# Kernel tuning notes

Hardware: AMD Instinct MI355X
Metric: run time of the kernel (lower is better)

The kernel has to match this reference:

```python
import jax, jax.numpy as jnp
import numpy as np

D_MODEL = 1024
N_HEADS = 16
D_K = D_MODEL // N_HEADS
BATCH = 4
SEQ = 2048


def setup_inputs() -> dict:
    key = jax.random.key(0)
    ks = jax.random.split(key, 9)
    s = 1.0 / np.sqrt(D_MODEL)
    x = jax.random.normal(ks[0], (BATCH, SEQ, D_MODEL), dtype=jnp.float32)
    # nn.Linear weights stored as [out, in]; we keep [in, out] for x @ W
    Wq = jax.random.uniform(ks[1], (D_MODEL, D_MODEL), jnp.float32, -s, s)
    bq = jax.random.uniform(ks[2], (D_MODEL,), jnp.float32, -s, s)
    Wk = jax.random.uniform(ks[3], (D_MODEL, D_MODEL), jnp.float32, -s, s)
    bk = jax.random.uniform(ks[4], (D_MODEL,), jnp.float32, -s, s)
    Wv = jax.random.uniform(ks[5], (D_MODEL, D_MODEL), jnp.float32, -s, s)
    bv = jax.random.uniform(ks[6], (D_MODEL,), jnp.float32, -s, s)
    Wo = jax.random.uniform(ks[7], (D_MODEL, D_MODEL), jnp.float32, -s, s)
    bo = jax.random.uniform(ks[8], (D_MODEL,), jnp.float32, -s, s)
    return {"x": x, "Wq": Wq, "bq": bq, "Wk": Wk, "bk": bk,
            "Wv": Wv, "bv": bv, "Wo": Wo, "bo": bo}


def reference(x, Wq, bq, Wk, bk, Wv, bv, Wo, bo):
    B, S, _ = x.shape
    # projections -> [B, H, S, d_k]
    def heads(t):
        return t.reshape(B, S, N_HEADS, D_K).transpose(0, 2, 1, 3)
    q = heads(x @ Wq + bq)
    k = heads(x @ Wk + bk)
    v = heads(x @ Wv + bv)
    scores = jnp.einsum('bhqd,bhkd->bhqk', q, k) / jnp.sqrt(jnp.float32(D_K))
    causal = jnp.tril(jnp.ones((S, S), dtype=bool))
    scores = jnp.where(causal[None, None], scores, -jnp.inf)
    attn = jax.nn.softmax(scores, axis=-1)  # dropout p=0 (eval) -> identity
    out = jnp.einsum('bhqk,bhkd->bhqd', attn, v)
    out = out.transpose(0, 2, 1, 3).reshape(B, S, D_MODEL)
    return out @ Wo + bo
```

## Files before the change

kernel.cpp:

```cpp
#include <hip/hip_runtime.h>
#include <hip/hip_bf16.h>
#include <stdint.h>

#define D_MODEL 1024
#define N_HEADS 16
#define D_KH    64
#define BATCH   4
#define SEQ     2048
#define M_TOTAL (BATCH * SEQ)

typedef unsigned short u16;
typedef short  bf16x8 __attribute__((ext_vector_type(8)));
typedef float  f32x4  __attribute__((ext_vector_type(4)));

__device__ __forceinline__ float bf2f(u16 u) {
    union { uint32_t i; float f; } c; c.i = ((uint32_t)u) << 16; return c.f;
}
__device__ __forceinline__ u16 f2bf(float f) {
    union { float f; uint32_t i; } c; c.f = f;
    uint32_t r = (c.i + 0x7FFFu + ((c.i >> 16) & 1u)) >> 16;
    return (u16)r;
}
__device__ __forceinline__ uint32_t cvt_pk_bf16(float lo, float hi) {
    uint32_t r;
    asm("v_cvt_pk_bf16_f32 %0, %1, %2" : "=v"(r) : "v"(lo), "v"(hi));
    return r;
}
__device__ __forceinline__ float sane(float v) {
    return (v == v && v > -1e30f && v < 1e30f) ? v : 0.f;
}
__device__ __forceinline__ float loadf(const void* base, size_t idx, int isbf) {
    return isbf ? bf2f(((const u16*)base)[idx]) : ((const float*)base)[idx];
}
__device__ __forceinline__ void gload16(const void* g, void* lds) {
    __builtin_amdgcn_global_load_lds(
        (const __attribute__((address_space(1))) void*)g,
        (__attribute__((address_space(3))) void*)lds, 16, 0, 0);
}

__global__ void detect_dtype(const uint32_t* __restrict__ w, int* __restrict__ flag) {
    uint32_t word = w[threadIdx.x & 63];
    uint32_t e = (word >> 7) & 0xFFu;
    unsigned long long m = __ballot(e >= 64u && e <= 160u);
    if (threadIdx.x == 0) *flag = (__popcll(m) >= 48) ? 1 : 0;
}

__global__ __launch_bounds__(256) void convert_x(
    const void* __restrict__ x, u16* __restrict__ dst, const int* __restrict__ flag)
{
    if (*flag) return;
    size_t i = ((size_t)blockIdx.x * 256 + threadIdx.x) * 8;
    const float* f = (const float*)x + i;
    float4 a = *(const float4*)f;
    float4 b = *(const float4*)(f + 4);
    union { ushort4 v; u16 s[4]; } lo, hi;
    lo.s[0] = f2bf(a.x); lo.s[1] = f2bf(a.y); lo.s[2] = f2bf(a.z); lo.s[3] = f2bf(a.w);
    hi.s[0] = f2bf(b.x); hi.s[1] = f2bf(b.y); hi.s[2] = f2bf(b.z); hi.s[3] = f2bf(b.w);
    *(ushort4*)&dst[i]     = lo.v;
    *(ushort4*)&dst[i + 4] = hi.v;
}

__global__ __launch_bounds__(256) void transpose_w(
    const void* __restrict__ W0, const void* __restrict__ W1,
    const void* __restrict__ W2, u16* __restrict__ dst,
    const int* __restrict__ flag)
{
    const int mat = blockIdx.z;
    const void* W = (mat == 0) ? W0 : ((mat == 1) ? W1 : W2);
    const int isbf = *flag;
    const int n0 = blockIdx.x << 6, k0 = blockIdx.y << 6;
    __shared__ u16 Ts[64 * 72];
    const int t = threadIdx.x;
    const int rr = t >> 4, cc = (t & 15) << 2;

#pragma unroll
    for (int i = 0; i < 4; i++) {
        int row = rr + i * 16;
        if (isbf) {
            ushort4 v = *(const ushort4*)((const u16*)W + (size_t)(k0 + row) * D_MODEL + n0 + cc);
            *(ushort4*)&Ts[row * 72 + cc] = v;
        } else {
            float4 f = *(const float4*)((const float*)W + (size_t)(k0 + row) * D_MODEL + n0 + cc);
            Ts[row * 72 + cc + 0] = f2bf(f.x);
            Ts[row * 72 + cc + 1] = f2bf(f.y);
            Ts[row * 72 + cc + 2] = f2bf(f.z);
            Ts[row * 72 + cc + 3] = f2bf(f.w);
        }
    }
    __syncthreads();
#pragma unroll
    for (int i = 0; i < 4; i++) {
        int n = rr + i * 16;
        union { ushort4 v; u16 s[4]; } o;
        o.s[0] = Ts[(cc + 0) * 72 + n];
        o.s[1] = Ts[(cc + 1) * 72 + n];
        o.s[2] = Ts[(cc + 2) * 72 + n];
        o.s[3] = Ts[(cc + 3) * 72 + n];
        *(ushort4*)&dst[(size_t)mat * 1048576 + (size_t)(n0 + n) * D_MODEL + k0 + cc] = o.v;
    }
}

__global__ __launch_bounds__(256) void qkv_gemm(
    const void* __restrict__ Xorig, const u16* __restrict__ Xbf,
    const u16* __restrict__ Wt,
    const void* __restrict__ bq, const void* __restrict__ bk, const void* __restrict__ bv,
    u16* __restrict__ Qd, u16* __restrict__ Kw, u16* __restrict__ Vt,
    const int* __restrict__ flag)
{
    const int isbf = *flag;
    const u16* Xp = isbf ? (const u16*)Xorig : Xbf;

    const int tid = threadIdx.x;
    const int wave = tid >> 6, lane = tid & 63;
    const int quad = lane >> 4, l15 = lane & 15;
    const int wr = wave >> 1, wc = wave & 1;

    const int nt  = blockIdx.x;
    const int mat = nt >> 3;
    const int n0m = (nt & 7) << 7;
    const int m0  = blockIdx.y << 7;

    const u16* Wmat = Wt + (size_t)mat * 1048576;
    const void* bias = (mat == 0) ? bq : ((mat == 1) ? bk : bv);

    __shared__ __align__(16) u16 As[128 * 36];
    __shared__ __align__(16) u16 Bs[128 * 36];

    f32x4 acc[4][4];
#pragma unroll
    for (int i = 0; i < 4; i++)
#pragma unroll
        for (int j = 0; j < 4; j++) acc[i][j] = (f32x4){0.f, 0.f, 0.f, 0.f};

    for (int k0 = 0; k0 < D_MODEL; k0 += 32) {
#pragma unroll
        for (int i = 0; i < 2; i++) {
            int c = tid + (i << 8);
            int row = c >> 2, koff = (c & 3) << 3;
            *(uint4*)&As[row * 36 + koff] =
                *(const uint4*)&Xp[(size_t)(m0 + row) * D_MODEL + k0 + koff];
            *(uint4*)&Bs[row * 36 + koff] =
                *(const uint4*)&Wmat[(size_t)(n0m + row) * D_MODEL + k0 + koff];
        }
        __syncthreads();

        bf16x8 af[4], bf[4];
#pragma unroll
        for (int ms = 0; ms < 4; ms++)
            af[ms] = *(const bf16x8*)&As[(wr * 64 + ms * 16 + l15) * 36 + quad * 8];
#pragma unroll
        for (int ns = 0; ns < 4; ns++)
            bf[ns] = *(const bf16x8*)&Bs[(wc * 64 + ns * 16 + l15) * 36 + quad * 8];
#pragma unroll
        for (int ms = 0; ms < 4; ms++)
#pragma unroll
            for (int ns = 0; ns < 4; ns++)
                acc[ms][ns] = __builtin_amdgcn_mfma_f32_16x16x32_bf16(af[ms], bf[ns], acc[ms][ns], 0, 0, 0);
        __syncthreads();
    }

#pragma unroll
    for (int ns = 0; ns < 4; ns++) {
        int c = n0m + wc * 64 + ns * 16 + l15;
        float bv_ = loadf(bias, c, isbf);
        int h = c >> 6, d = c & 63;
#pragma unroll
        for (int ms = 0; ms < 4; ms++) {
            int rbase = m0 + wr * 64 + ms * 16 + quad * 4;
            int b = rbase >> 11;
            int sbase = rbase & 2047;
            int bh = b * N_HEADS + h;
            if (mat == 2) {
                union { ushort4 v; u16 s[4]; } o;
#pragma unroll
                for (int r = 0; r < 4; r++) o.s[r] = f2bf(sane(acc[ms][ns][r] + bv_));
                *(ushort4*)&Vt[((size_t)bh * D_KH + d) * SEQ + sbase] = o.v;
            } else {
                u16* Out = (mat == 0) ? Qd : Kw;
#pragma unroll
                for (int r = 0; r < 4; r++)
                    Out[((size_t)bh * SEQ + sbase + r) * D_KH + d] =
                        f2bf(sane(acc[ms][ns][r] + bv_));
            }
        }
    }
}

__global__ __launch_bounds__(256, 2) void attn_kernel(
    const u16* __restrict__ Qd, const u16* __restrict__ Kw,
    const u16* __restrict__ Vt, u16* __restrict__ Aw)
{
    const int tid = threadIdx.x;
    const int wave = tid >> 6, lane = tid & 63;
    const int quad = lane >> 4, l15 = lane & 15;

    const int bh = blockIdx.x;
    const int p  = blockIdx.y;
    const int b  = bh >> 4, h = bh & 15;

    const u16* Qb = Qd + (size_t)bh * SEQ * D_KH;
    const char* Kb = (const char*)(Kw + (size_t)bh * SEQ * D_KH);
    const char* Vb = (const char*)(Vt + (size_t)bh * D_KH * SEQ);

    __shared__ __align__(16) u16 KV[2][8192];
    __shared__ __align__(16) u16 Ps[4][32 * 64];
    char* Pw = (char*)Ps[wave];

    const float CEXP = 0.18033688011112042f;

    const int lrow = lane >> 3;
    const int gchk = (lane & 7) ^ lrow;
    const int hxor = l15 & 7;

    for (int ph = 0; ph < 2; ph++) {
        const int qt = ph ? (15 - p) : p;
        const int qrow0 = qt * 128 + wave * 32;

        bf16x8 qf[2][2];
#pragma unroll
        for (int qs = 0; qs < 2; qs++) {
            const u16* qrow = Qb + (size_t)(qrow0 + qs * 16 + l15) * D_KH + quad * 8;
            qf[qs][0] = *(const bf16x8*)(qrow);
            qf[qs][1] = *(const bf16x8*)(qrow + 32);
        }

        float mi[2], li[2];
        f32x4 od[4][2];
        mi[0] = mi[1] = -1e9f; li[0] = li[1] = 0.f;
#pragma unroll
        for (int db = 0; db < 4; db++)
#pragma unroll
            for (int qs = 0; qs < 2; qs++) od[db][qs] = (f32x4){0.f, 0.f, 0.f, 0.f};

        const int ktn = 2 * qt + 2;

        auto stage_issue = [&](int k0, int buf) {
            char* kb = (char*)KV[buf];
#pragma unroll
            for (int j = 0; j < 2; j++) {
                const int r0 = 16 * wave + 8 * j;
                gload16(Kb + (size_t)(k0 + r0 + lrow) * 128 + 16 * gchk,
                        kb + r0 * 128);
                gload16(Vb + (size_t)(r0 + lrow) * 4096 + (size_t)k0 * 2 + 16 * gchk,
                        kb + 8192 + r0 * 128);
            }
        };

        stage_issue(0, 0);
        __syncthreads();

        int cur = 0;
        for (int kt = 0; kt < ktn; ++kt) {
            const int k0 = kt << 6;
            const bool pf = (kt + 1 < ktn);

            if (pf) stage_issue(k0 + 64, cur ^ 1);

            const char* kb = (const char*)KV[cur];

            bf16x8 kf[4][2];
#pragma unroll
            for (int nb = 0; nb < 4; nb++) {
                const char* kr = kb + (nb * 16 + l15) * 128;
                kf[nb][0] = *(const bf16x8*)(kr + 16 * (quad ^ hxor));
                kf[nb][1] = *(const bf16x8*)(kr + 16 * ((4 + quad) ^ hxor));
            }

            f32x4 st[4][2];
#pragma unroll
            for (int nb = 0; nb < 4; nb++)
#pragma unroll
                for (int qs = 0; qs < 2; qs++) {
                    f32x4 t = (f32x4){0.f, 0.f, 0.f, 0.f};
                    t = __builtin_amdgcn_mfma_f32_16x16x32_bf16(kf[nb][0], qf[qs][0], t, 0, 0, 0);
                    t = __builtin_amdgcn_mfma_f32_16x16x32_bf16(kf[nb][1], qf[qs][1], t, 0, 0, 0);
                    st[nb][qs] = t;
                }

            if (kt >= 2 * qt) {
#pragma unroll
                for (int qs = 0; qs < 2; qs++) {
                    const int q = qrow0 + qs * 16 + l15;
#pragma unroll
                    for (int nb = 0; nb < 4; nb++) {
                        const int kb0 = k0 + nb * 16 + quad * 4;
#pragma unroll
                        for (int r = 0; r < 4; r++)
                            if (kb0 + r > q) st[nb][qs][r] = -1e9f;
                    }
                }
            }

#pragma unroll
            for (int qs = 0; qs < 2; qs++) {
                float a0 = fmaxf(fmaxf(st[0][qs][0], st[0][qs][1]), fmaxf(st[0][qs][2], st[0][qs][3]));
                float a1 = fmaxf(fmaxf(st[1][qs][0], st[1][qs][1]), fmaxf(st[1][qs][2], st[1][qs][3]));
                float a2 = fmaxf(fmaxf(st[2][qs][0], st[2][qs][1]), fmaxf(st[2][qs][2], st[2][qs][3]));
                float a3 = fmaxf(fmaxf(st[3][qs][0], st[3][qs][1]), fmaxf(st[3][qs][2], st[3][qs][3]));
                float pmax = fmaxf(fmaxf(a0, a1), fmaxf(a2, a3));
                pmax = fmaxf(pmax, __shfl_xor(pmax, 16, 64));
                pmax = fmaxf(pmax, __shfl_xor(pmax, 32, 64));
                if (__any(pmax > mi[qs] + 8.0f)) {
                    float mnew  = fmaxf(mi[qs], pmax);
                    float alpha = exp2f((mi[qs] - mnew) * CEXP);
                    mi[qs] = mnew;
                    li[qs] *= alpha;
#pragma unroll
                    for (int db = 0; db < 4; db++) {
                        od[db][qs][0] *= alpha; od[db][qs][1] *= alpha;
                        od[db][qs][2] *= alpha; od[db][qs][3] *= alpha;
                    }
                }
                const float mc = mi[qs] * CEXP;
                float srow_ = 0.f;
#pragma unroll
                for (int nb = 0; nb < 4; nb++) {
                    float pf0 = exp2f(fmaf(st[nb][qs][0], CEXP, -mc));
                    float pf1 = exp2f(fmaf(st[nb][qs][1], CEXP, -mc));
                    float pf2 = exp2f(fmaf(st[nb][qs][2], CEXP, -mc));
                    float pf3 = exp2f(fmaf(st[nb][qs][3], CEXP, -mc));
                    srow_ += (pf0 + pf1) + (pf2 + pf3);
                    union { uint2 w; ushort4 v; } pk;
                    pk.w.x = cvt_pk_bf16(pf0, pf1);
                    pk.w.y = cvt_pk_bf16(pf2, pf3);
                    const int sw = (4 * nb + quad) ^ ((l15 & 7) << 1);
                    *(uint2*)(Pw + (qs * 16 + l15) * 128 + sw * 8) = pk.w;
                }
                srow_ += __shfl_xor(srow_, 16, 64);
                srow_ += __shfl_xor(srow_, 32, 64);
                li[qs] += srow_;
            }

            bf16x8 pa[2][2];
#pragma unroll
            for (int qs = 0; qs < 2; qs++)
#pragma unroll
                for (int j = 0; j < 2; j++) {
                    const int mw = (4 * j + quad) ^ (l15 & 7);
                    pa[qs][j] = *(const bf16x8*)(Pw + (qs * 16 + l15) * 128 + mw * 16);
                }

#pragma unroll
            for (int db = 0; db < 4; db++) {
                const char* vr = kb + 8192 + (db * 16 + l15) * 128;
                bf16x8 v0 = *(const bf16x8*)(vr + 16 * (quad ^ hxor));
                bf16x8 v1 = *(const bf16x8*)(vr + 16 * ((4 + quad) ^ hxor));
#pragma unroll
                for (int qs = 0; qs < 2; qs++) {
                    od[db][qs] = __builtin_amdgcn_mfma_f32_16x16x32_bf16(v0, pa[qs][0], od[db][qs], 0, 0, 0);
                    od[db][qs] = __builtin_amdgcn_mfma_f32_16x16x32_bf16(v1, pa[qs][1], od[db][qs], 0, 0, 0);
                }
            }

            __syncthreads();
            cur ^= 1;
        }

#pragma unroll
        for (int qs = 0; qs < 2; qs++) {
            const int q = qrow0 + qs * 16 + l15;
            const float inv = 1.0f / fmaxf(li[qs], 1e-30f);
            u16* orow = Aw + (size_t)(b * SEQ + q) * D_MODEL + h * D_KH;
#pragma unroll
            for (int db = 0; db < 4; db++)
#pragma unroll
                for (int r = 0; r < 4; r++)
                    orow[db * 16 + quad * 4 + r] = f2bf(sane(od[db][qs][r] * inv));
        }
        __syncthreads();
    }
}

__global__ __launch_bounds__(256) void out_gemm(
    const u16* __restrict__ A, const u16* __restrict__ Wot,
    const void* __restrict__ bias, void* __restrict__ Out,
    const int* __restrict__ flag)
{
    const int isbf = *flag;
    const int tid = threadIdx.x;
    const int wave = tid >> 6, lane = tid & 63;
    const int quad = lane >> 4, l15 = lane & 15;
    const int wr = wave >> 1, wc = wave & 1;

    const int n0 = blockIdx.x << 7;
    const int m0 = blockIdx.y << 7;

    __shared__ __align__(16) u16 As[128 * 36];
    __shared__ __align__(16) u16 Bs[128 * 36];

    f32x4 acc[4][4];
#pragma unroll
    for (int i = 0; i < 4; i++)
#pragma unroll
        for (int j = 0; j < 4; j++) acc[i][j] = (f32x4){0.f, 0.f, 0.f, 0.f};

    for (int k0 = 0; k0 < D_MODEL; k0 += 32) {
#pragma unroll
        for (int i = 0; i < 2; i++) {
            int c = tid + (i << 8);
            int row = c >> 2, koff = (c & 3) << 3;
            *(uint4*)&As[row * 36 + koff] =
                *(const uint4*)&A[(size_t)(m0 + row) * D_MODEL + k0 + koff];
            *(uint4*)&Bs[row * 36 + koff] =
                *(const uint4*)&Wot[(size_t)(n0 + row) * D_MODEL + k0 + koff];
        }
        __syncthreads();

        bf16x8 af[4], bf[4];
#pragma unroll
        for (int ms = 0; ms < 4; ms++)
            af[ms] = *(const bf16x8*)&As[(wr * 64 + ms * 16 + l15) * 36 + quad * 8];
#pragma unroll
        for (int ns = 0; ns < 4; ns++)
            bf[ns] = *(const bf16x8*)&Bs[(wc * 64 + ns * 16 + l15) * 36 + quad * 8];
#pragma unroll
        for (int ms = 0; ms < 4; ms++)
#pragma unroll
            for (int ns = 0; ns < 4; ns++)
                acc[ms][ns] = __builtin_amdgcn_mfma_f32_16x16x32_bf16(af[ms], bf[ns], acc[ms][ns], 0, 0, 0);
        __syncthreads();
    }

#pragma unroll
    for (int ns = 0; ns < 4; ns++) {
        int col = n0 + wc * 64 + ns * 16 + l15;
        float bv_ = loadf(bias, col, isbf);
#pragma unroll
        for (int ms = 0; ms < 4; ms++) {
#pragma unroll
            for (int r = 0; r < 4; r++) {
                int row = m0 + wr * 64 + ms * 16 + quad * 4 + r;
                float v = sane(acc[ms][ns][r] + bv_);
                size_t idx = (size_t)row * D_MODEL + col;
                if (isbf) ((u16*)Out)[idx] = f2bf(v);
                else      ((float*)Out)[idx] = v;
            }
        }
    }
}

__global__ void zero_out_kernel(void* out, int n, const int* flag) {
    int i = blockIdx.x * 256 + threadIdx.x;
    if (i < n) {
        if (*flag) ((u16*)out)[i] = 0;
        else       ((float*)out)[i] = 0.f;
    }
}

extern "C" void kernel_launch(void* const* d_in, const int* in_sizes, int n_in,
                              void* d_out, int out_size, void* d_ws, size_t ws_size,
                              hipStream_t stream)
{
    const void* x  = d_in[0];
    const void* Wq = d_in[1];
    const void* bq = d_in[2];
    const void* Wk = d_in[3];
    const void* bk = d_in[4];
    const void* Wv = d_in[5];
    const void* bv = d_in[6];
    const void* Wo = d_in[7];
    const void* bo = d_in[8];

    const size_t NELT = (size_t)M_TOTAL * D_MODEL;
    const size_t HDR  = 4096;
    const size_t NEED = HDR + 3 * NELT * sizeof(u16);

    int* flag = (int*)d_ws;
    detect_dtype<<<1, 64, 0, stream>>>((const uint32_t*)Wq, flag);

    if (ws_size < NEED) {
        zero_out_kernel<<<(out_size + 255) / 256, 256, 0, stream>>>(d_out, out_size, flag);
        return;
    }

    u16* base = (u16*)((char*)d_ws + HDR);
    u16* Kw      = base;
    u16* Vt      = base + NELT;
    u16* Wo_t    = Vt;
    u16* Wqkv_t  = base + 2 * NELT;
    u16* Aw      = base + 2 * NELT;
    u16* Qd      = (u16*)d_out;
    u16* Xbf     = (u16*)d_out + NELT;

    convert_x<<<dim3(M_TOTAL * D_MODEL / (8 * 256)), 256, 0, stream>>>(x, Xbf, flag);
    transpose_w<<<dim3(16, 16, 3), 256, 0, stream>>>(Wq, Wk, Wv, Wqkv_t, flag);

    qkv_gemm<<<dim3(24, 64), 256, 0, stream>>>(x, Xbf, Wqkv_t, bq, bk, bv,
                                               Qd, Kw, Vt, flag);
    attn_kernel<<<dim3(64, 8), 256, 0, stream>>>(Qd, Kw, Vt, Aw);
    transpose_w<<<dim3(16, 16, 1), 256, 0, stream>>>(Wo, Wo, Wo, Wo_t, flag);
    out_gemm<<<dim3(8, 64), 256, 0, stream>>>(Aw, Wo_t, bo, d_out, flag);
}
```

Baseline: 313.5 us.

## Double-buffer GEMM tiles with direct global-to-LDS loads and XOR swizzle

Both the QKV and output-projection GEMMs now use a double-buffered LDS pipeline with a K-tile of 64. The next tile is fetched with gload16 (global-to-LDS loads) while MFMAs run on the current one, and an XOR swizzle replaces the padded layout to avoid bank conflicts. This removes one barrier per step and the register round-trip for staging, aiming to overlap memory latency with compute. The cost is LDS use rising to 64KB per block, and the launch bound now asks for 2 blocks per CU.

```diff
diff --git a/kernel.cpp b/kernel.cpp
--- a/kernel.cpp
+++ b/kernel.cpp
@@ -100,7 +100,7 @@
     }
 }
 
-__global__ __launch_bounds__(256) void qkv_gemm(
+__global__ __launch_bounds__(256, 2) void qkv_gemm(
     const void* __restrict__ Xorig, const u16* __restrict__ Xbf,
     const u16* __restrict__ Wt,
     const void* __restrict__ bq, const void* __restrict__ bk, const void* __restrict__ bv,
@@ -123,8 +123,25 @@
     const u16* Wmat = Wt + (size_t)mat * 1048576;
     const void* bias = (mat == 0) ? bq : ((mat == 1) ? bk : bv);
 
-    __shared__ __align__(16) u16 As[128 * 36];
-    __shared__ __align__(16) u16 Bs[128 * 36];
+    __shared__ __align__(16) u16 As[2][128 * 64];
+    __shared__ __align__(16) u16 Bs[2][128 * 64];
+
+    const int lrow = lane >> 3;
+    const int gchk = (lane & 7) ^ lrow;
+    const int hxor = l15 & 7;
+
+    auto stage = [&](int k0, int buf) {
+        char* ap = (char*)As[buf];
+        char* bp = (char*)Bs[buf];
+#pragma unroll
+        for (int j = 0; j < 4; j++) {
+            const int r0 = 32 * wave + 8 * j;
+            gload16((const char*)Xp   + ((size_t)(m0  + r0 + lrow) * D_MODEL + k0) * 2 + 16 * gchk,
+                    ap + r0 * 128);
+            gload16((const char*)Wmat + ((size_t)(n0m + r0 + lrow) * D_MODEL + k0) * 2 + 16 * gchk,
+                    bp + r0 * 128);
+        }
+    };
 
     f32x4 acc[4][4];
 #pragma unroll
@@ -132,31 +149,36 @@
 #pragma unroll
         for (int j = 0; j < 4; j++) acc[i][j] = (f32x4){0.f, 0.f, 0.f, 0.f};
 
-    for (int k0 = 0; k0 < D_MODEL; k0 += 32) {
-#pragma unroll
-        for (int i = 0; i < 2; i++) {
-            int c = tid + (i << 8);
-            int row = c >> 2, koff = (c & 3) << 3;
-            *(uint4*)&As[row * 36 + koff] =
-                *(const uint4*)&Xp[(size_t)(m0 + row) * D_MODEL + k0 + koff];
-            *(uint4*)&Bs[row * 36 + koff] =
-                *(const uint4*)&Wmat[(size_t)(n0m + row) * D_MODEL + k0 + koff];
+    stage(0, 0);
+    __syncthreads();
+
+    int cur = 0;
+    for (int kt = 0; kt < 16; ++kt) {
+        if (kt + 1 < 16) stage((kt + 1) * 64, cur ^ 1);
+
+        const char* ap = (const char*)As[cur];
+        const char* bp = (const char*)Bs[cur];
+#pragma unroll
+        for (int kk = 0; kk < 2; kk++) {
+            bf16x8 af[4], bf[4];
+#pragma unroll
+            for (int ms = 0; ms < 4; ms++) {
+                const char* ar = ap + (wr * 64 + ms * 16 + l15) * 128;
+                af[ms] = *(const bf16x8*)(ar + 16 * ((4 * kk + quad) ^ hxor));
+            }
+#pragma unroll
+            for (int ns = 0; ns < 4; ns++) {
+                const char* br = bp + (wc * 64 + ns * 16 + l15) * 128;
+                bf[ns] = *(const bf16x8*)(br + 16 * ((4 * kk + quad) ^ hxor));
+            }
+#pragma unroll
+            for (int ms = 0; ms < 4; ms++)
+#pragma unroll
+                for (int ns = 0; ns < 4; ns++)
+                    acc[ms][ns] = __builtin_amdgcn_mfma_f32_16x16x32_bf16(af[ms], bf[ns], acc[ms][ns], 0, 0, 0);
         }
         __syncthreads();
-
-        bf16x8 af[4], bf[4];
-#pragma unroll
-        for (int ms = 0; ms < 4; ms++)
-            af[ms] = *(const bf16x8*)&As[(wr * 64 + ms * 16 + l15) * 36 + quad * 8];
-#pragma unroll
-        for (int ns = 0; ns < 4; ns++)
-            bf[ns] = *(const bf16x8*)&Bs[(wc * 64 + ns * 16 + l15) * 36 + quad * 8];
-#pragma unroll
-        for (int ms = 0; ms < 4; ms++)
-#pragma unroll
-            for (int ns = 0; ns < 4; ns++)
-                acc[ms][ns] = __builtin_amdgcn_mfma_f32_16x16x32_bf16(af[ms], bf[ns], acc[ms][ns], 0, 0, 0);
-        __syncthreads();
+        cur ^= 1;
     }
 
 #pragma unroll
@@ -371,7 +393,7 @@
     }
 }
 
-__global__ __launch_bounds__(256) void out_gemm(
+__global__ __launch_bounds__(256, 2) void out_gemm(
     const u16* __restrict__ A, const u16* __restrict__ Wot,
     const void* __restrict__ bias, void* __restrict__ Out,
     const int* __restrict__ flag)
@@ -385,8 +407,25 @@
     const int n0 = blockIdx.x << 7;
     const int m0 = blockIdx.y << 7;
 
-    __shared__ __align__(16) u16 As[128 * 36];
-    __shared__ __align__(16) u16 Bs[128 * 36];
+    __shared__ __align__(16) u16 As[2][128 * 64];
+    __shared__ __align__(16) u16 Bs[2][128 * 64];
+
+    const int lrow = lane >> 3;
+    const int gchk = (lane & 7) ^ lrow;
+    const int hxor = l15 & 7;
+
+    auto stage = [&](int k0, int buf) {
+        char* ap = (char*)As[buf];
+        char* bp = (char*)Bs[buf];
+#pragma unroll
+        for (int j = 0; j < 4; j++) {
+            const int r0 = 32 * wave + 8 * j;
+            gload16((const char*)A   + ((size_t)(m0 + r0 + lrow) * D_MODEL + k0) * 2 + 16 * gchk,
+                    ap + r0 * 128);
+            gload16((const char*)Wot + ((size_t)(n0 + r0 + lrow) * D_MODEL + k0) * 2 + 16 * gchk,
+                    bp + r0 * 128);
+        }
+    };
 
     f32x4 acc[4][4];
 #pragma unroll
@@ -394,31 +433,36 @@
 #pragma unroll
         for (int j = 0; j < 4; j++) acc[i][j] = (f32x4){0.f, 0.f, 0.f, 0.f};
 
-    for (int k0 = 0; k0 < D_MODEL; k0 += 32) {
-#pragma unroll
-        for (int i = 0; i < 2; i++) {
-            int c = tid + (i << 8);
-            int row = c >> 2, koff = (c & 3) << 3;
-            *(uint4*)&As[row * 36 + koff] =
-                *(const uint4*)&A[(size_t)(m0 + row) * D_MODEL + k0 + koff];
-            *(uint4*)&Bs[row * 36 + koff] =
-                *(const uint4*)&Wot[(size_t)(n0 + row) * D_MODEL + k0 + koff];
+    stage(0, 0);
+    __syncthreads();
+
+    int cur = 0;
+    for (int kt = 0; kt < 16; ++kt) {
+        if (kt + 1 < 16) stage((kt + 1) * 64, cur ^ 1);
+
+        const char* ap = (const char*)As[cur];
+        const char* bp = (const char*)Bs[cur];
+#pragma unroll
+        for (int kk = 0; kk < 2; kk++) {
+            bf16x8 af[4], bf[4];
+#pragma unroll
+            for (int ms = 0; ms < 4; ms++) {
+                const char* ar = ap + (wr * 64 + ms * 16 + l15) * 128;
+                af[ms] = *(const bf16x8*)(ar + 16 * ((4 * kk + quad) ^ hxor));
+            }
+#pragma unroll
+            for (int ns = 0; ns < 4; ns++) {
+                const char* br = bp + (wc * 64 + ns * 16 + l15) * 128;
+                bf[ns] = *(const bf16x8*)(br + 16 * ((4 * kk + quad) ^ hxor));
+            }
+#pragma unroll
+            for (int ms = 0; ms < 4; ms++)
+#pragma unroll
+                for (int ns = 0; ns < 4; ns++)
+                    acc[ms][ns] = __builtin_amdgcn_mfma_f32_16x16x32_bf16(af[ms], bf[ns], acc[ms][ns], 0, 0, 0);
         }
         __syncthreads();
-
-        bf16x8 af[4], bf[4];
-#pragma unroll
-        for (int ms = 0; ms < 4; ms++)
-            af[ms] = *(const bf16x8*)&As[(wr * 64 + ms * 16 + l15) * 36 + quad * 8];
-#pragma unroll
-        for (int ns = 0; ns < 4; ns++)
-            bf[ns] = *(const bf16x8*)&Bs[(wc * 64 + ns * 16 + l15) * 36 + quad * 8];
-#pragma unroll
-        for (int ms = 0; ms < 4; ms++)
-#pragma unroll
-            for (int ns = 0; ns < 4; ns++)
-                acc[ms][ns] = __builtin_amdgcn_mfma_f32_16x16x32_bf16(af[ms], bf[ns], acc[ms][ns], 0, 0, 0);
-        __syncthreads();
+        cur ^= 1;
     }
 
 #pragma unroll
```

New measurement: 281.6 us. 1.11x faster.
